# Kernel tuning notes

Hardware: AMD Instinct MI355X
Metric: run time of the kernel (lower is better)

Reference implementation:

```python
import jax, jax.numpy as jnp
import numpy as np

B = 4096
N_FEAT = 4
VOCAB = 100000
EMB = 64
N_NEG = 3
TEMP = 1.0
EPS = 1e-8  # torch.cosine_similarity eps


def setup_inputs() -> dict:
    key = jax.random.key(0)
    ks = jax.random.split(key, 12)
    inp = {}
    inp['user_ids'] = jax.random.randint(ks[0], (B, N_FEAT), 0, VOCAB)
    inp['item_ids'] = jax.random.randint(ks[1], (B, N_FEAT), 0, VOCAB)
    inp['sw_ids'] = jax.random.randint(ks[2], (B,), 0, VOCAB)
    inp['user_tables'] = jax.random.normal(ks[3], (N_FEAT, VOCAB, EMB), jnp.float32) * 0.05
    inp['item_tables'] = jax.random.normal(ks[4], (N_FEAT, VOCAB, EMB), jnp.float32) * 0.05
    # sample weights must be positive (log is taken)
    inp['sw_table'] = jax.random.uniform(ks[5], (VOCAB,), jnp.float32) * 0.99 + 0.01
    inp['uW1'] = jax.random.normal(ks[6], (256, 256), jnp.float32) * 0.05
    inp['ub1'] = jnp.zeros((256,), jnp.float32)
    inp['uW2'] = jax.random.normal(ks[7], (256, 128), jnp.float32) * 0.05
    inp['ub2'] = jnp.zeros((128,), jnp.float32)
    inp['iW1'] = jax.random.normal(ks[8], (256, 256), jnp.float32) * 0.05
    inp['ib1'] = jnp.zeros((256,), jnp.float32)
    inp['iW2'] = jax.random.normal(ks[9], (256, 128), jnp.float32) * 0.05
    inp['ib2'] = jnp.zeros((128,), jnp.float32)
    return inp


def _embed(tables, ids):
    # tables: [F, V, E], ids: [B, F] -> [B, F*E]
    e = jax.vmap(lambda tbl, idx: tbl[idx], in_axes=(0, 1))(tables, ids)  # [F, B, E]
    return jnp.transpose(e, (1, 0, 2)).reshape(ids.shape[0], -1)


def _mlp(x, W1, b1, W2, b2):
    # torch-rechub MLP with output_layer=False: activation after every layer
    h = jax.nn.relu(x @ W1 + b1)
    return jax.nn.relu(h @ W2 + b2)


def reference(user_ids, item_ids, sw_ids, user_tables, item_tables, sw_table,
              uW1, ub1, uW2, ub2, iW1, ib1, iW2, ib2):
    u = _mlp(_embed(user_tables, user_ids), uW1, ub1, uW2, ub2)   # [B, 128]
    v = _mlp(_embed(item_tables, item_ids), iW1, ib1, iW2, ib2)   # [B, 128]
    un = u / jnp.maximum(jnp.linalg.norm(u, axis=-1, keepdims=True), EPS)
    vn = v / jnp.maximum(jnp.linalg.norm(v, axis=-1, keepdims=True), EPS)
    pred = un @ vn.T                                              # [B, B] cosine sim
    sw = sw_table[sw_ids]                                         # [B]
    scores = pred - jnp.log(sw)[None, :]                          # debias per item column
    # in-batch negative sampling: row i pairs with cols (i..i+n_neg) mod B
    rows = jnp.repeat(jnp.arange(B), N_NEG + 1)
    cols = ((jnp.arange(B)[:, None] + jnp.arange(N_NEG + 1)[None, :]) % B).reshape(-1)
    out = scores[rows, cols] / TEMP
    return out.reshape(B, N_NEG + 1)
```

## Files before the change

### kernel.cpp

```cpp
#include <hip/hip_runtime.h>
#include <math.h>

#define BATCH 4096
#define NFEAT 4
#define VOCAB 100000
#define EMB 64
#define D_IN 256
#define D_H 256
#define D_O 128
#define ROWS 16
#define XS_STRIDE 264
#define YS_STRIDE 132

typedef __attribute__((ext_vector_type(8))) short bf16x8;
typedef __attribute__((ext_vector_type(4))) float f32x4;

__device__ inline ushort f2bf(float f) {
  union { float f; unsigned u; } v; v.f = f;
  unsigned u = v.u;
  return (ushort)((u + 0x7fffu + ((u >> 16) & 1u)) >> 16);
}

__device__ inline bf16x8 load_wfrag(const float* __restrict__ wp, int strideN) {
  bf16x8 b;
#pragma unroll
  for (int j = 0; j < 8; j++) b[j] = (short)f2bf(wp[(size_t)j * strideN]);
  return b;
}

__global__ __launch_bounds__(256) void tower_kernel(
    const int* __restrict__ user_ids, const int* __restrict__ item_ids,
    const float* __restrict__ user_tables, const float* __restrict__ item_tables,
    const float* __restrict__ uW1, const float* __restrict__ ub1,
    const float* __restrict__ uW2, const float* __restrict__ ub2,
    const float* __restrict__ iW1, const float* __restrict__ ib1,
    const float* __restrict__ iW2, const float* __restrict__ ib2,
    float* __restrict__ U, float* __restrict__ V) {
  const int tower = blockIdx.y;
  const int* ids = tower ? item_ids : user_ids;
  const float* tab = tower ? item_tables : user_tables;
  const float* W1 = tower ? iW1 : uW1;
  const float* b1 = tower ? ib1 : ub1;
  const float* W2 = tower ? iW2 : uW2;
  const float* b2 = tower ? ib2 : ub2;
  float* O = tower ? V : U;

  const int r0 = blockIdx.x * ROWS;
  const int tid = threadIdx.x;

  __shared__ ushort Xs[ROWS][XS_STRIDE];
  __shared__ ushort Hs[ROWS][XS_STRIDE];
  __shared__ float Ys[ROWS][YS_STRIDE];

#pragma unroll
  for (int i = 0; i < 4; i++) {
    int slot = i * 256 + tid;
    int row = slot >> 6;
    int c4 = slot & 63;
    int f = c4 >> 4;
    int id = ids[(size_t)(r0 + row) * NFEAT + f];
    float4 v = ((const float4*)(tab + ((size_t)f * VOCAB + (size_t)id) * EMB))[c4 & 15];
    ushort4 o = {f2bf(v.x), f2bf(v.y), f2bf(v.z), f2bf(v.w)};
    *(ushort4*)&Xs[row][c4 * 4] = o;
  }
  __syncthreads();

  const int lane = tid & 63;
  const int w = tid >> 6;
  const int m = lane & 15;
  const int quad = lane >> 4;

  {
    bf16x8 a[8];
#pragma unroll
    for (int k0 = 0; k0 < 8; k0++)
      a[k0] = *(const bf16x8*)&Xs[m][k0 * 32 + quad * 8];
#pragma unroll
    for (int ct = 0; ct < 4; ct++) {
      int n = (w * 4 + ct) * 16 + m;
      const float* wp = W1 + (size_t)(quad * 8) * D_H + n;
      f32x4 acc = {0.f, 0.f, 0.f, 0.f};
#pragma unroll
      for (int k0 = 0; k0 < 8; k0++)
        acc = __builtin_amdgcn_mfma_f32_16x16x32_bf16(
            a[k0], load_wfrag(wp + (size_t)k0 * 32 * D_H, D_H), acc, 0, 0, 0);
      float bias = b1[n];
#pragma unroll
      for (int reg = 0; reg < 4; reg++) {
        int r = quad * 4 + reg;
        Hs[r][n] = f2bf(fmaxf(acc[reg] + bias, 0.f));
      }
    }
  }
  __syncthreads();

  {
    bf16x8 h[8];
#pragma unroll
    for (int k0 = 0; k0 < 8; k0++)
      h[k0] = *(const bf16x8*)&Hs[m][k0 * 32 + quad * 8];
#pragma unroll
    for (int ct = 0; ct < 2; ct++) {
      int n = (w * 2 + ct) * 16 + m;
      const float* wp = W2 + (size_t)(quad * 8) * D_O + n;
      f32x4 acc = {0.f, 0.f, 0.f, 0.f};
#pragma unroll
      for (int k0 = 0; k0 < 8; k0++)
        acc = __builtin_amdgcn_mfma_f32_16x16x32_bf16(
            h[k0], load_wfrag(wp + (size_t)k0 * 32 * D_O, D_O), acc, 0, 0, 0);
      float bias = b2[n];
#pragma unroll
      for (int reg = 0; reg < 4; reg++) {
        int r = quad * 4 + reg;
        Ys[r][n] = fmaxf(acc[reg] + bias, 0.f);
      }
    }
  }
  __syncthreads();

#pragma unroll
  for (int rr = 0; rr < 4; rr++) {
    int row = w * 4 + rr;
    float y0 = Ys[row][lane];
    float y1 = Ys[row][64 + lane];
    float s = y0 * y0 + y1 * y1;
#pragma unroll
    for (int off = 32; off; off >>= 1) s += __shfl_xor(s, off);
    float inv = 1.f / fmaxf(sqrtf(s), 1e-8f);
    float* op = O + (size_t)(r0 + row) * D_O;
    op[lane] = y0 * inv;
    op[64 + lane] = y1 * inv;
  }
}

__global__ __launch_bounds__(256) void score_kernel(
    const float* __restrict__ U, const float* __restrict__ V,
    const int* __restrict__ sw_ids, const float* __restrict__ sw_table,
    float* __restrict__ out) {
  int wave = threadIdx.x >> 6;
  int lane = threadIdx.x & 63;
  int i = blockIdx.x * 4 + wave;

  float u0 = U[(size_t)i * D_O + lane];
  float u1 = U[(size_t)i * D_O + 64 + lane];

#pragma unroll
  for (int j = 0; j < 4; j++) {
    int c = (i + j) & (BATCH - 1);
    float v0 = V[(size_t)c * D_O + lane];
    float v1 = V[(size_t)c * D_O + 64 + lane];
    float d = u0 * v0 + u1 * v1;
#pragma unroll
    for (int off = 32; off; off >>= 1) d += __shfl_xor(d, off);
    if (lane == 0) {
      out[(size_t)i * 4 + j] = d - logf(sw_table[sw_ids[c]]);
    }
  }
}

extern "C" void kernel_launch(void* const* d_in, const int* in_sizes, int n_in,
                              void* d_out, int out_size, void* d_ws, size_t ws_size,
                              hipStream_t stream) {
  (void)in_sizes; (void)n_in; (void)out_size; (void)ws_size;
  const int*   user_ids    = (const int*)d_in[0];
  const int*   item_ids    = (const int*)d_in[1];
  const int*   sw_ids      = (const int*)d_in[2];
  const float* user_tables = (const float*)d_in[3];
  const float* item_tables = (const float*)d_in[4];
  const float* sw_table    = (const float*)d_in[5];
  const float* uW1 = (const float*)d_in[6];
  const float* ub1 = (const float*)d_in[7];
  const float* uW2 = (const float*)d_in[8];
  const float* ub2 = (const float*)d_in[9];
  const float* iW1 = (const float*)d_in[10];
  const float* ib1 = (const float*)d_in[11];
  const float* iW2 = (const float*)d_in[12];
  const float* ib2 = (const float*)d_in[13];
  float* out = (float*)d_out;

  float* U = (float*)d_ws;
  float* V = U + (size_t)BATCH * D_O;

  tower_kernel<<<dim3(BATCH / ROWS, 2), 256, 0, stream>>>(
      user_ids, item_ids, user_tables, item_tables,
      uW1, ub1, uW2, ub2, iW1, ib1, iW2, ib2, U, V);

  score_kernel<<<BATCH / 4, 256, 0, stream>>>(U, V, sw_ids, sw_table, out);
}
```

Measured before the change: 218.3 us.

## Fuse both towers and scoring into one kernel with halo item rows

Measured after the change: 226.0 us. 1.04x slower.

```diff
diff --git a/kernel.cpp b/kernel.cpp
--- a/kernel.cpp
+++ b/kernel.cpp
@@ -8,7 +8,6 @@
 #define D_IN 256
 #define D_H 256
 #define D_O 128
-#define ROWS 16
 #define XS_STRIDE 264
 #define YS_STRIDE 132
 
@@ -28,132 +27,142 @@
   return b;
 }
 
-__global__ __launch_bounds__(256) void tower_kernel(
+__global__ __launch_bounds__(512) void fused_kernel(
     const int* __restrict__ user_ids, const int* __restrict__ item_ids,
+    const int* __restrict__ sw_ids,
     const float* __restrict__ user_tables, const float* __restrict__ item_tables,
+    const float* __restrict__ sw_table,
     const float* __restrict__ uW1, const float* __restrict__ ub1,
     const float* __restrict__ uW2, const float* __restrict__ ub2,
     const float* __restrict__ iW1, const float* __restrict__ ib1,
     const float* __restrict__ iW2, const float* __restrict__ ib2,
-    float* __restrict__ U, float* __restrict__ V) {
-  const int tower = blockIdx.y;
-  const int* ids = tower ? item_ids : user_ids;
-  const float* tab = tower ? item_tables : user_tables;
-  const float* W1 = tower ? iW1 : uW1;
-  const float* b1 = tower ? ib1 : ub1;
-  const float* W2 = tower ? iW2 : uW2;
-  const float* b2 = tower ? ib2 : ub2;
-  float* O = tower ? V : U;
+    float* __restrict__ out) {
+  const int r0 = blockIdx.x * 16;
+  const int tid = threadIdx.x;
+  const int lane = tid & 63;
+  const int w = tid >> 6;
 
-  const int r0 = blockIdx.x * ROWS;
-  const int tid = threadIdx.x;
+  __shared__ ushort Xs_u[16][XS_STRIDE];
+  __shared__ ushort Xs_i[32][XS_STRIDE];
+  __shared__ ushort Hs_u[16][XS_STRIDE];
+  __shared__ ushort Hs_i[32][XS_STRIDE];
+  __shared__ float Ys_u[16][YS_STRIDE];
+  __shared__ float Ys_i[32][YS_STRIDE];
 
-  __shared__ ushort Xs[ROWS][XS_STRIDE];
-  __shared__ ushort Hs[ROWS][XS_STRIDE];
-  __shared__ float Ys[ROWS][YS_STRIDE];
-
-#pragma unroll
-  for (int i = 0; i < 4; i++) {
-    int slot = i * 256 + tid;
-    int row = slot >> 6;
-    int c4 = slot & 63;
+  for (int s = tid; s < 2240; s += 512) {
+    bool isu = s < 1024;
+    int t = isu ? s : s - 1024;
+    int row = t >> 6;
+    int c4 = t & 63;
     int f = c4 >> 4;
-    int id = ids[(size_t)(r0 + row) * NFEAT + f];
+    int grow = (r0 + row) & (BATCH - 1);
+    const int* ids = isu ? user_ids : item_ids;
+    const float* tab = isu ? user_tables : item_tables;
+    int id = ids[(size_t)grow * NFEAT + f];
     float4 v = ((const float4*)(tab + ((size_t)f * VOCAB + (size_t)id) * EMB))[c4 & 15];
     ushort4 o = {f2bf(v.x), f2bf(v.y), f2bf(v.z), f2bf(v.w)};
-    *(ushort4*)&Xs[row][c4 * 4] = o;
+    if (isu) *(ushort4*)&Xs_u[row][c4 * 4] = o;
+    else     *(ushort4*)&Xs_i[row][c4 * 4] = o;
+  }
+  for (int z = tid; z < 13 * 66; z += 512) {
+    int row = 19 + z / 66, c = z % 66;
+    ushort4 zz = {0, 0, 0, 0};
+    *(ushort4*)&Xs_i[row][c * 4] = zz;
   }
   __syncthreads();
 
-  const int lane = tid & 63;
-  const int w = tid >> 6;
   const int m = lane & 15;
   const int quad = lane >> 4;
 
-  {
+#pragma unroll
+  for (int s = 0; s < 6; s++) {
+    int t = w * 6 + s;
+    int tile = t >> 4;
+    int ct = t & 15;
+    const ushort (*X)[XS_STRIDE] = tile == 0 ? Xs_u : (tile == 1 ? Xs_i : Xs_i + 16);
+    ushort (*H)[XS_STRIDE] = tile == 0 ? Hs_u : (tile == 1 ? Hs_i : Hs_i + 16);
+    const float* Wm = tile == 0 ? uW1 : iW1;
+    const float* bm = tile == 0 ? ub1 : ib1;
     bf16x8 a[8];
 #pragma unroll
     for (int k0 = 0; k0 < 8; k0++)
-      a[k0] = *(const bf16x8*)&Xs[m][k0 * 32 + quad * 8];
+      a[k0] = *(const bf16x8*)&X[m][k0 * 32 + quad * 8];
+    int n = ct * 16 + m;
+    const float* wp = Wm + (size_t)(quad * 8) * D_H + n;
+    f32x4 acc = {0.f, 0.f, 0.f, 0.f};
 #pragma unroll
-    for (int ct = 0; ct < 4; ct++) {
-      int n = (w * 4 + ct) * 16 + m;
-      const float* wp = W1 + (size_t)(quad * 8) * D_H + n;
-      f32x4 acc = {0.f, 0.f, 0.f, 0.f};
+    for (int k0 = 0; k0 < 8; k0++)
+      acc = __builtin_amdgcn_mfma_f32_16x16x32_bf16(
+          a[k0], load_wfrag(wp + (size_t)k0 * 32 * D_H, D_H), acc, 0, 0, 0);
+    float bias = bm[n];
 #pragma unroll
-      for (int k0 = 0; k0 < 8; k0++)
-        acc = __builtin_amdgcn_mfma_f32_16x16x32_bf16(
-            a[k0], load_wfrag(wp + (size_t)k0 * 32 * D_H, D_H), acc, 0, 0, 0);
-      float bias = b1[n];
-#pragma unroll
-      for (int reg = 0; reg < 4; reg++) {
-        int r = quad * 4 + reg;
-        Hs[r][n] = f2bf(fmaxf(acc[reg] + bias, 0.f));
-      }
-    }
+    for (int reg = 0; reg < 4; reg++)
+      H[quad * 4 + reg][n] = f2bf(fmaxf(acc[reg] + bias, 0.f));
   }
   __syncthreads();
 
-  {
+#pragma unroll
+  for (int s = 0; s < 3; s++) {
+    int t = w * 3 + s;
+    int tile = t >> 3;
+    int ct = t & 7;
+    const ushort (*H)[XS_STRIDE] = tile == 0 ? Hs_u : (tile == 1 ? Hs_i : Hs_i + 16);
+    float (*Y)[YS_STRIDE] = tile == 0 ? Ys_u : (tile == 1 ? Ys_i : Ys_i + 16);
+    const float* Wm = tile == 0 ? uW2 : iW2;
+    const float* bm = tile == 0 ? ub2 : ib2;
     bf16x8 h[8];
 #pragma unroll
     for (int k0 = 0; k0 < 8; k0++)
-      h[k0] = *(const bf16x8*)&Hs[m][k0 * 32 + quad * 8];
+      h[k0] = *(const bf16x8*)&H[m][k0 * 32 + quad * 8];
+    int n = ct * 16 + m;
+    const float* wp = Wm + (size_t)(quad * 8) * D_O + n;
+    f32x4 acc = {0.f, 0.f, 0.f, 0.f};
 #pragma unroll
-    for (int ct = 0; ct < 2; ct++) {
-      int n = (w * 2 + ct) * 16 + m;
-      const float* wp = W2 + (size_t)(quad * 8) * D_O + n;
-      f32x4 acc = {0.f, 0.f, 0.f, 0.f};
+    for (int k0 = 0; k0 < 8; k0++)
+      acc = __builtin_amdgcn_mfma_f32_16x16x32_bf16(
+          h[k0], load_wfrag(wp + (size_t)k0 * 32 * D_O, D_O), acc, 0, 0, 0);
+    float bias = bm[n];
 #pragma unroll
-      for (int k0 = 0; k0 < 8; k0++)
-        acc = __builtin_amdgcn_mfma_f32_16x16x32_bf16(
-            h[k0], load_wfrag(wp + (size_t)k0 * 32 * D_O, D_O), acc, 0, 0, 0);
-      float bias = b2[n];
+    for (int reg = 0; reg < 4; reg++)
+      Y[quad * 4 + reg][n] = fmaxf(acc[reg] + bias, 0.f);
+  }
+  __syncthreads();
+
 #pragma unroll
-      for (int reg = 0; reg < 4; reg++) {
-        int r = quad * 4 + reg;
-        Ys[r][n] = fmaxf(acc[reg] + bias, 0.f);
-      }
+  for (int rr = 0; rr < 5; rr++) {
+    int row = rr * 8 + w;
+    if (row < 35) {
+      float* Y = row < 16 ? &Ys_u[row][0] : &Ys_i[row - 16][0];
+      float y0 = Y[lane];
+      float y1 = Y[64 + lane];
+      float s2 = y0 * y0 + y1 * y1;
+#pragma unroll
+      for (int off = 32; off; off >>= 1) s2 += __shfl_xor(s2, off);
+      float inv = 1.f / fmaxf(sqrtf(s2), 1e-8f);
+      Y[lane] = y0 * inv;
+      Y[64 + lane] = y1 * inv;
     }
   }
   __syncthreads();
 
 #pragma unroll
-  for (int rr = 0; rr < 4; rr++) {
-    int row = w * 4 + rr;
-    float y0 = Ys[row][lane];
-    float y1 = Ys[row][64 + lane];
-    float s = y0 * y0 + y1 * y1;
+  for (int rr = 0; rr < 2; rr++) {
+    int il = w * 2 + rr;
+    int i = r0 + il;
+    float u0 = Ys_u[il][lane];
+    float u1 = Ys_u[il][64 + lane];
 #pragma unroll
-    for (int off = 32; off; off >>= 1) s += __shfl_xor(s, off);
-    float inv = 1.f / fmaxf(sqrtf(s), 1e-8f);
-    float* op = O + (size_t)(r0 + row) * D_O;
-    op[lane] = y0 * inv;
-    op[64 + lane] = y1 * inv;
-  }
-}
-
-__global__ __launch_bounds__(256) void score_kernel(
-    const float* __restrict__ U, const float* __restrict__ V,
-    const int* __restrict__ sw_ids, const float* __restrict__ sw_table,
-    float* __restrict__ out) {
-  int wave = threadIdx.x >> 6;
-  int lane = threadIdx.x & 63;
-  int i = blockIdx.x * 4 + wave;
-
-  float u0 = U[(size_t)i * D_O + lane];
-  float u1 = U[(size_t)i * D_O + 64 + lane];
-
+    for (int j = 0; j < 4; j++) {
+      int cl = il + j;
+      float v0 = Ys_i[cl][lane];
+      float v1 = Ys_i[cl][64 + lane];
+      float d = u0 * v0 + u1 * v1;
 #pragma unroll
-  for (int j = 0; j < 4; j++) {
-    int c = (i + j) & (BATCH - 1);
-    float v0 = V[(size_t)c * D_O + lane];
-    float v1 = V[(size_t)c * D_O + 64 + lane];
-    float d = u0 * v0 + u1 * v1;
-#pragma unroll
-    for (int off = 32; off; off >>= 1) d += __shfl_xor(d, off);
-    if (lane == 0) {
-      out[(size_t)i * 4 + j] = d - logf(sw_table[sw_ids[c]]);
+      for (int off = 32; off; off >>= 1) d += __shfl_xor(d, off);
+      if (lane == 0) {
+        int c = (i + j) & (BATCH - 1);
+        out[(size_t)i * 4 + j] = d - logf(sw_table[sw_ids[c]]);
+      }
     }
   }
 }
@@ -161,7 +170,7 @@
 extern "C" void kernel_launch(void* const* d_in, const int* in_sizes, int n_in,
                               void* d_out, int out_size, void* d_ws, size_t ws_size,
                               hipStream_t stream) {
-  (void)in_sizes; (void)n_in; (void)out_size; (void)ws_size;
+  (void)in_sizes; (void)n_in; (void)out_size; (void)d_ws; (void)ws_size;
   const int*   user_ids    = (const int*)d_in[0];
   const int*   item_ids    = (const int*)d_in[1];
   const int*   sw_ids      = (const int*)d_in[2];
@@ -178,12 +187,7 @@
   const float* ib2 = (const float*)d_in[13];
   float* out = (float*)d_out;
 
-  float* U = (float*)d_ws;
-  float* V = U + (size_t)BATCH * D_O;
-
-  tower_kernel<<<dim3(BATCH / ROWS, 2), 256, 0, stream>>>(
-      user_ids, item_ids, user_tables, item_tables,
-      uW1, ub1, uW2, ub2, iW1, ib1, iW2, ib2, U, V);
-
-  score_kernel<<<BATCH / 4, 256, 0, stream>>>(U, V, sw_ids, sw_table, out);
+  fused_kernel<<<BATCH / 16, 512, 0, stream>>>(
+      user_ids, item_ids, sw_ids, user_tables, item_tables, sw_table,
+      uW1, ub1, uW2, ub2, iW1, ib1, iW2, ib2, out);
 }
```
